# Performance work log

Hardware: AMD Instinct MI355X
Metric: run time of the kernel (lower is better)

## Reference

```python
import jax, jax.numpy as jnp
import numpy as np

B, T, C, H, W = 4, 5, 512, 32, 32   # bt = B*T = 20
G = 32                              # GroupNorm groups
EPS = 1e-6


def group_norm(x, gamma, beta):
    # x: [N, C, H, W]; normalize per (group-channels, H, W)
    n, c, h, w = x.shape
    xg = x.reshape(n, G, c // G, h * w)
    mu = jnp.mean(xg, axis=(2, 3), keepdims=True)
    var = jnp.mean((xg - mu) ** 2, axis=(2, 3), keepdims=True)
    xn = ((xg - mu) * jax.lax.rsqrt(var + EPS)).reshape(n, c, h, w)
    return xn * gamma[None, :, None, None] + beta[None, :, None, None]


def conv1x1(x, w, b):
    # 1x1 conv == channel matmul. x: [N,C,H,W], w: [O,C], b: [O]
    return jnp.einsum('nchw,oc->nohw', x, w) + b[None, :, None, None]


def setup_inputs() -> dict:
    key = jax.random.key(0)
    ks = jax.random.split(key, 9)
    inp = {'x': jax.random.normal(ks[0], (B * T, C, H, W), jnp.float32)}
    for i, nm in enumerate(['wq', 'wk', 'wv', 'wo', 'wqt', 'wkt', 'wvt', 'wot']):
        inp[nm] = jax.random.normal(ks[i + 1], (C, C), jnp.float32) * 0.02
        inp['b' + nm[1:]] = jnp.zeros((C,), jnp.float32)
    inp['gamma_s'] = jnp.ones((C,), jnp.float32)
    inp['beta_s'] = jnp.zeros((C,), jnp.float32)
    inp['gamma_t'] = jnp.ones((C,), jnp.float32)
    inp['beta_t'] = jnp.zeros((C,), jnp.float32)
    return inp


def reference(x, wq, bq, wk, bk, wv, bv, wo, bo,
              wqt, bqt, wkt, bkt, wvt, bvt, wot, bot,
              gamma_s, beta_s, gamma_t, beta_t):
    scale = float(C) ** -0.5

    # ---- spatial attention (AttnBlock.forward) ----
    hn = group_norm(x, gamma_s, beta_s)
    q = conv1x1(hn, wq, bq).reshape(B * T, C, H * W)
    k = conv1x1(hn, wk, bk).reshape(B * T, C, H * W)
    v = conv1x1(hn, wv, bv).reshape(B * T, C, H * W)
    # scores [bt, hw_q, hw_k], softmax over keys
    att = jax.nn.softmax(jnp.einsum('bcq,bck->bqk', q, k) * scale, axis=2)
    hsp = jnp.einsum('bck,bqk->bcq', v, att).reshape(B * T, C, H, W)
    spatio = x + conv1x1(hsp, wo, bo)

    # ---- temporal attention across t=5 frames per pixel ----
    hn = group_norm(spatio, gamma_t, beta_t)
    q5 = conv1x1(hn, wqt, bqt).reshape(B, T, C, H, W)
    k5 = conv1x1(hn, wkt, bkt).reshape(B, T, C, H, W)
    v5 = conv1x1(hn, wvt, bvt).reshape(B, T, C, H, W)
    # per-pixel [t, t] attention, softmax over key-frame axis s
    att_t = jax.nn.softmax(jnp.einsum('btchw,bschw->bhwts', q5, k5) * scale, axis=-1)
    htp = jnp.einsum('bhwts,bschw->btchw', att_t, v5).reshape(B * T, C, H, W)

    # NOTE: residual is the ORIGINAL x (faithful to the source), not spatio
    return x + conv1x1(htp, wot, bot)
```

## Files before the change

### kernel.cpp

```cpp
#include <hip/hip_runtime.h>
#include <hip/hip_bf16.h>
#include <stdint.h>

typedef unsigned short u16;
typedef __attribute__((ext_vector_type(8))) short bf16x8;
typedef __attribute__((ext_vector_type(4))) float f32x4;

#define DI __device__ __forceinline__

DI float b2f(u16 u) { return __uint_as_float(((uint32_t)u) << 16); }
DI u16 f2b(float f) {
  uint32_t u = __float_as_uint(f);
  u += 0x7fff + ((u >> 16) & 1);
  return (u16)(u >> 16);
}

DI void gld_lds16(const u16* g, u16* l) {
  __builtin_amdgcn_global_load_lds((const __attribute__((address_space(1))) void*)g,
                                   (__attribute__((address_space(3))) void*)l,
                                   16, 0, 0);
}

__global__ __launch_bounds__(256)
void setup_wb(const float* __restrict__ w0, const float* __restrict__ w1,
              const float* __restrict__ w2, const float* __restrict__ w3,
              const float* __restrict__ w4, const float* __restrict__ w5,
              const float* __restrict__ w6, const float* __restrict__ w7,
              const float* __restrict__ b0, const float* __restrict__ b1,
              const float* __restrict__ b2, const float* __restrict__ b3,
              const float* __restrict__ b4, const float* __restrict__ b5,
              const float* __restrict__ b6, const float* __restrict__ b7,
              u16* __restrict__ dst, float* __restrict__ bdst)
{
  if (blockIdx.x >= 1032) {
    const int a = (blockIdx.x - 1032) * 256 + threadIdx.x;
    float acc = 0.f;
    for (int c = 0; c < 512; ++c) acc += w3[a * 512 + c] * b2[c];
    bdst[4096 + a] = acc;
    return;
  }
  if (blockIdx.x >= 1024) {
    const float* bs[8] = {b0, b1, b2, b3, b4, b5, b6, b7};
    const int a = blockIdx.x - 1024;
    const int i = threadIdx.x;
    bdst[a * 512 + i] = bs[a][i];
    bdst[a * 512 + i + 256] = bs[a][i + 256];
    return;
  }
  const float* srcs[8] = {w0, w1, w2, w3, w4, w5, w6, w7};
  const int mat = blockIdx.x >> 7;
  const int i = (((blockIdx.x & 127) << 8) + threadIdx.x) * 8;
  const float* s = srcs[mat];
  float4 a = *(const float4*)(s + i);
  float4 b = *(const float4*)(s + i + 4);
  alignas(16) u16 v[8] = {f2b(a.x), f2b(a.y), f2b(a.z), f2b(a.w),
                          f2b(b.x), f2b(b.y), f2b(b.z), f2b(b.w)};
  *(uint4*)(dst + (long)mat * 262144 + i) = *(const uint4*)v;
  if (mat == 2) {
    const int row = i >> 9, col = i & 511;
#pragma unroll
    for (int j = 0; j < 8; ++j) dst[8 * 262144 + (col + j) * 512 + row] = v[j];
  }
}

template<int OUTF32, int BIASMODE, int RESID>
__global__ __launch_bounds__(256)
void gemm_bt(const u16* __restrict__ A, long sA, long lda,
             const u16* __restrict__ B, long sB, long ldb,
             void* __restrict__ C, long sC,
             const float* __restrict__ bias,
             const float* __restrict__ resid, long sR,
             int N, int K, float alpha)
{
  __shared__ u16 lA[2 * 128 * 32];
  __shared__ u16 lB[2 * 128 * 32];
  const int t = threadIdx.x;
  const int lane = t & 63;
  const int wid = t >> 6;

  const int nx = gridDim.x;
  const int bid = blockIdx.y * nx + blockIdx.x;
  const int nper = (nx * gridDim.y) >> 3;
  const int nid = (bid & 7) * nper + (bid >> 3);
  const int m0 = (nid / nx) * 128, n0 = (nid % nx) * 128;

  const long bz = blockIdx.z;
  const u16* Ab = A + bz * sA;
  const u16* Bb = B + bz * sB;

  const int row = t >> 2;
  const int kc  = (((t & 3) ^ ((t >> 3) & 3)) << 3);

  f32x4 acc[4][4];
#pragma unroll
  for (int i = 0; i < 4; ++i)
#pragma unroll
    for (int j = 0; j < 4; ++j) acc[i][j] = (f32x4){0.f, 0.f, 0.f, 0.f};

  const int ml = lane & 15, qd = lane >> 4;
  const int koff = ((qd ^ ((ml >> 1) & 3)) << 3);
  const int wm = (wid >> 1) * 64, wn = (wid & 1) * 64;

  auto stage = [&](int bsel, int k0) {
    const u16* Ap = Ab + (long)(m0 + row) * lda + (k0 + kc);
    const u16* Bp = Bb + (long)(n0 + row) * ldb + (k0 + kc);
    u16* la = lA + bsel * 4096 + wid * 512;
    u16* lb = lB + bsel * 4096 + wid * 512;
    gld_lds16(Ap, la);
    gld_lds16(Ap + 64 * lda, la + 2048);
    gld_lds16(Bp, lb);
    gld_lds16(Bp + 64 * ldb, lb + 2048);
  };

  const int niter = K >> 5;
  stage(0, 0);
  for (int i = 0; i < niter; ++i) {
    __syncthreads();
    if (i + 1 < niter) stage((i + 1) & 1, (i + 1) << 5);
    const u16* la = lA + (i & 1) * 4096;
    const u16* lb = lB + (i & 1) * 4096;
    bf16x8 af[4], bfr[4];
#pragma unroll
    for (int x = 0; x < 4; ++x)
      af[x] = *(const bf16x8*)&la[(wm + x * 16 + ml) * 32 + koff];
#pragma unroll
    for (int y = 0; y < 4; ++y)
      bfr[y] = *(const bf16x8*)&lb[(wn + y * 16 + ml) * 32 + koff];
#pragma unroll
    for (int x = 0; x < 4; ++x)
#pragma unroll
      for (int y = 0; y < 4; ++y)
        acc[x][y] = __builtin_amdgcn_mfma_f32_16x16x32_bf16(af[x], bfr[y], acc[x][y], 0, 0, 0);
  }

  const long cb = bz * sC;
#pragma unroll
  for (int i = 0; i < 4; ++i) {
#pragma unroll
    for (int j = 0; j < 4; ++j) {
#pragma unroll
      for (int r = 0; r < 4; ++r) {
        int rr = m0 + wm + i * 16 + qd * 4 + r;
        int cc = n0 + wn + j * 16 + ml;
        float v = acc[i][j][r] * alpha;
        if (BIASMODE == 1) v += bias[rr];
        if (BIASMODE == 2) v += bias[cc];
        long idx = (long)rr * N + cc;
        if (RESID) v += resid[bz * sR + idx];
        if (OUTF32) ((float*)C)[cb + idx] = v;
        else        ((u16*)C)[cb + idx] = f2b(v);
      }
    }
  }
}

template<int OUTF32, int BIASMODE, int RESID>
__global__ __launch_bounds__(512, 2)
void gemm256(const u16* __restrict__ A, long sA, long lda,
             const u16* __restrict__ B, long sB, long ldb,
             void* __restrict__ C, long sC,
             const float* __restrict__ bias,
             const float* __restrict__ resid, long sR,
             int N, int K, float alpha)
{
  __shared__ u16 lA[4 * 8192];
  __shared__ u16 lB[4 * 8192];
  const int t = threadIdx.x;
  const int lane = t & 63, wid = t >> 6;
  const int wr = wid >> 2, wc = wid & 3;
  const int ml = lane & 15, qd = lane >> 4;

  const int nx = gridDim.x;
  const int bid = blockIdx.y * nx + blockIdx.x;
  const int nper = (nx * gridDim.y) >> 3;
  const int nid = (bid & 7) * nper + (bid >> 3);
  const int m0 = (nid / nx) * 256, n0 = (nid % nx) * 256;

  const long bz = blockIdx.z;
  const u16* Ab = A + bz * sA;
  const u16* Bb = B + bz * sB;

  const int sw = ((lane & 3) ^ ((lane >> 3) & 3)) << 3;
  const int srow = wid * 32 + (lane >> 2);
  const u16* ApS = Ab + (long)(m0 + srow) * lda + sw;
  const u16* BpS = Bb + (long)(n0 + srow) * ldb + sw;
  u16* lwA = lA + wid * 1024;
  u16* lwB = lB + wid * 1024;

  f32x4 acc[8][4];
#pragma unroll
  for (int i = 0; i < 8; ++i)
#pragma unroll
    for (int j = 0; j < 4; ++j) acc[i][j] = (f32x4){0.f, 0.f, 0.f, 0.f};

  const int NT = K >> 5;

  auto stageA = [&](int tk) {
    const int bo = (tk & 3) << 13;
    const u16* p = ApS + ((long)tk << 5);
    gld_lds16(p,              lwA + bo);
    gld_lds16(p + (lda << 4), lwA + bo + 512);
  };
  auto stageB = [&](int tk) {
    const int bo = (tk & 3) << 13;
    const u16* p = BpS + ((long)tk << 5);
    gld_lds16(p,              lwB + bo);
    gld_lds16(p + (ldb << 4), lwB + bo + 512);
  };

  const int koff = (qd ^ ((ml >> 1) & 3)) << 3;
  const int rAo = (wr * 128 + ml) * 32 + koff;
  const int rBo = (wc * 64 + ml) * 32 + koff;

  stageA(0); stageB(0); stageA(1); stageB(1); stageA(2); stageB(2);
  asm volatile("s_waitcnt vmcnt(8)" ::: "memory");
  __builtin_amdgcn_s_barrier();
  __builtin_amdgcn_sched_barrier(0);

  for (int tk = 0; tk < NT; ++tk) {
    const int bo = (tk & 3) << 13;
    const u16* pa = lA + bo + rAo;
    const u16* pb = lB + bo + rBo;
    bf16x8 bfr[4], af[4];

#pragma unroll
    for (int n = 0; n < 4; ++n) bfr[n] = *(const bf16x8*)(pb + n * 512);
#pragma unroll
    for (int m = 0; m < 4; ++m) af[m] = *(const bf16x8*)(pa + m * 512);
    if (tk + 3 < NT) stageA(tk + 3);
    __builtin_amdgcn_sched_barrier(0);
    __builtin_amdgcn_s_barrier();
    asm volatile("s_waitcnt lgkmcnt(0)" ::: "memory");
    __builtin_amdgcn_sched_barrier(0);
    __builtin_amdgcn_s_setprio(1);
#pragma unroll
    for (int m = 0; m < 4; ++m)
#pragma unroll
      for (int n = 0; n < 4; ++n)
        acc[m][n] = __builtin_amdgcn_mfma_f32_16x16x32_bf16(af[m], bfr[n], acc[m][n], 0, 0, 0);
    __builtin_amdgcn_s_setprio(0);
    __builtin_amdgcn_sched_barrier(0);
    __builtin_amdgcn_s_barrier();
    __builtin_amdgcn_sched_barrier(0);

#pragma unroll
    for (int m = 0; m < 4; ++m) af[m] = *(const bf16x8*)(pa + (m + 4) * 512);
    if (tk + 3 < NT) stageB(tk + 3);
    __builtin_amdgcn_sched_barrier(0);
    __builtin_amdgcn_s_barrier();
    asm volatile("s_waitcnt lgkmcnt(0)" ::: "memory");
    __builtin_amdgcn_sched_barrier(0);
    __builtin_amdgcn_s_setprio(1);
#pragma unroll
    for (int m = 0; m < 4; ++m)
#pragma unroll
      for (int n = 0; n < 4; ++n)
        acc[m + 4][n] = __builtin_amdgcn_mfma_f32_16x16x32_bf16(af[m], bfr[n], acc[m + 4][n], 0, 0, 0);
    __builtin_amdgcn_s_setprio(0);
    __builtin_amdgcn_sched_barrier(0);

    if (tk < NT - 1) {
      const int rem = NT - 2 - tk;
      if (rem >= 2)      asm volatile("s_waitcnt vmcnt(8)" ::: "memory");
      else if (rem == 1) asm volatile("s_waitcnt vmcnt(4)" ::: "memory");
      else               asm volatile("s_waitcnt vmcnt(0)" ::: "memory");
      __builtin_amdgcn_s_barrier();
      __builtin_amdgcn_sched_barrier(0);
    }
  }

  const long cb = bz * sC;
#pragma unroll
  for (int mt = 0; mt < 8; ++mt) {
#pragma unroll
    for (int nt = 0; nt < 4; ++nt) {
#pragma unroll
      for (int r = 0; r < 4; ++r) {
        int rr = m0 + wr * 128 + mt * 16 + qd * 4 + r;
        int cc = n0 + wc * 64 + nt * 16 + ml;
        float v = acc[mt][nt][r] * alpha;
        if (BIASMODE == 1) v += bias[rr];
        if (BIASMODE == 2) v += bias[cc];
        long idx = (long)rr * N + cc;
        if (RESID) v += resid[bz * sR + idx];
        if (OUTF32) ((float*)C)[cb + idx] = v;
        else        ((u16*)C)[cb + idx] = f2b(v);
      }
    }
  }
}

__global__ __launch_bounds__(256)
void groupnorm_f32(const float* __restrict__ x, const float* __restrict__ gamma,
                   const float* __restrict__ beta, u16* __restrict__ out)
{
  const int C = 512, HW = 1024;
  const int n = blockIdx.x >> 5, g = blockIdx.x & 31;
  const float* xg = x + ((long)n * C + g * 16) * HW;
  const int t = threadIdx.x;
  float s = 0.f, ss = 0.f;
  for (int ch = t; ch < 4096; ch += 256) {
    float4 u = *(const float4*)(xg + ch * 4);
    s += u.x + u.y + u.z + u.w;
    ss += u.x * u.x + u.y * u.y + u.z * u.z + u.w * u.w;
  }
#pragma unroll
  for (int off = 32; off > 0; off >>= 1) { s += __shfl_xor(s, off); ss += __shfl_xor(ss, off); }
  __shared__ float rs[4], rss[4];
  if ((t & 63) == 0) { rs[t >> 6] = s; rss[t >> 6] = ss; }
  __syncthreads();
  s  = rs[0] + rs[1] + rs[2] + rs[3];
  ss = rss[0] + rss[1] + rss[2] + rss[3];
  const float mu = s * (1.f / 16384.f);
  const float var = ss * (1.f / 16384.f) - mu * mu;
  const float rstd = rsqrtf(var + 1e-6f);
  float gm[16], bt[16];
#pragma unroll
  for (int i = 0; i < 16; ++i) {
    float ga = gamma[g * 16 + i];
    gm[i] = ga * rstd;
    bt[i] = beta[g * 16 + i] - mu * ga * rstd;
  }
  for (int p = t; p < 1024; p += 256) {
    alignas(16) u16 vals[16];
#pragma unroll
    for (int i = 0; i < 16; ++i)
      vals[i] = f2b(xg[(long)i * HW + p] * gm[i] + bt[i]);
    u16* dst = out + ((long)n * HW + p) * C + g * 16;
    *(uint4*)dst       = *(const uint4*)&vals[0];
    *(uint4*)(dst + 8) = *(const uint4*)&vals[8];
  }
}

__global__ __launch_bounds__(256)
void groupnorm_bf16(const u16* __restrict__ x, const float* __restrict__ gamma,
                    const float* __restrict__ beta, u16* __restrict__ out)
{
  const int C = 512, HW = 1024;
  const int n = blockIdx.x >> 5, g = blockIdx.x & 31;
  const u16* xg = x + ((long)n * C + g * 16) * HW;
  const int t = threadIdx.x;
  float s = 0.f, ss = 0.f;
  for (int ch = t; ch < 2048; ch += 256) {
    uint4 u = *(const uint4*)(xg + ch * 8);
    uint32_t w[4] = {u.x, u.y, u.z, u.w};
#pragma unroll
    for (int k = 0; k < 4; ++k) {
      float f0 = __uint_as_float(w[k] << 16);
      float f1 = __uint_as_float(w[k] & 0xffff0000u);
      s += f0 + f1; ss += f0 * f0 + f1 * f1;
    }
  }
#pragma unroll
  for (int off = 32; off > 0; off >>= 1) { s += __shfl_xor(s, off); ss += __shfl_xor(ss, off); }
  __shared__ float rs[4], rss[4];
  if ((t & 63) == 0) { rs[t >> 6] = s; rss[t >> 6] = ss; }
  __syncthreads();
  s  = rs[0] + rs[1] + rs[2] + rs[3];
  ss = rss[0] + rss[1] + rss[2] + rss[3];
  const float mu = s * (1.f / 16384.f);
  const float var = ss * (1.f / 16384.f) - mu * mu;
  const float rstd = rsqrtf(var + 1e-6f);
  float gm[16], bt[16];
#pragma unroll
  for (int i = 0; i < 16; ++i) {
    float ga = gamma[g * 16 + i];
    gm[i] = ga * rstd;
    bt[i] = beta[g * 16 + i] - mu * ga * rstd;
  }
  for (int p = t; p < 1024; p += 256) {
    alignas(16) u16 vals[16];
#pragma unroll
    for (int i = 0; i < 16; ++i)
      vals[i] = f2b(b2f(xg[(long)i * HW + p]) * gm[i] + bt[i]);
    u16* dst = out + ((long)n * HW + p) * C + g * 16;
    *(uint4*)dst       = *(const uint4*)&vals[0];
    *(uint4*)(dst + 8) = *(const uint4*)&vals[8];
  }
}

__global__ __launch_bounds__(256)
void softmax1024(u16* __restrict__ data)
{
  u16* row = data + (long)blockIdx.x * 1024;
  const int t = threadIdx.x;
  uint2 u = *(const uint2*)(row + t * 4);
  float v[4];
  v[0] = __uint_as_float(u.x << 16); v[1] = __uint_as_float(u.x & 0xffff0000u);
  v[2] = __uint_as_float(u.y << 16); v[3] = __uint_as_float(u.y & 0xffff0000u);
  float mx = fmaxf(fmaxf(v[0], v[1]), fmaxf(v[2], v[3]));
#pragma unroll
  for (int off = 32; off > 0; off >>= 1) mx = fmaxf(mx, __shfl_xor(mx, off));
  __shared__ float red[8];
  if ((t & 63) == 0) red[t >> 6] = mx;
  __syncthreads();
  mx = fmaxf(fmaxf(red[0], red[1]), fmaxf(red[2], red[3]));
  float e[4]; float s = 0.f;
#pragma unroll
  for (int k = 0; k < 4; ++k) { e[k] = __expf(v[k] - mx); s += e[k]; }
#pragma unroll
  for (int off = 32; off > 0; off >>= 1) s += __shfl_xor(s, off);
  if ((t & 63) == 0) red[4 + (t >> 6)] = s;
  __syncthreads();
  s = red[4] + red[5] + red[6] + red[7];
  float inv = 1.f / s;
  uint2 o;
  o.x = (uint32_t)f2b(e[0] * inv) | ((uint32_t)f2b(e[1] * inv) << 16);
  o.y = (uint32_t)f2b(e[2] * inv) | ((uint32_t)f2b(e[3] * inv) << 16);
  *(uint2*)(row + t * 4) = o;
}

__global__ __launch_bounds__(256)
void temporal_attn(const u16* __restrict__ qkv, u16* __restrict__ htp)
{
  const int t = threadIdx.x;
  const int wv = t >> 6, lane = t & 63;
  const int pix = blockIdx.x * 4 + wv;
  const int b = pix >> 10, p = pix & 1023;
  const long fs = 1024l * 1536;
  const long rowbase = ((long)b * 5 * 1024 + p) * 1536 + lane * 8;

  float qf[5][8], kf[5][8];
#pragma unroll
  for (int f = 0; f < 5; ++f) {
    bf16x8 qv = *(const bf16x8*)(qkv + rowbase + f * fs);
    bf16x8 kv = *(const bf16x8*)(qkv + rowbase + f * fs + 512);
#pragma unroll
    for (int u = 0; u < 8; ++u) { qf[f][u] = b2f((u16)qv[u]); kf[f][u] = b2f((u16)kv[u]); }
  }
  float sc[25];
#pragma unroll
  for (int i = 0; i < 5; ++i)
#pragma unroll
    for (int j = 0; j < 5; ++j) {
      float a = 0.f;
#pragma unroll
      for (int u = 0; u < 8; ++u) a += qf[i][u] * kf[j][u];
      sc[i * 5 + j] = a;
    }
#pragma unroll
  for (int m = 1; m < 64; m <<= 1)
#pragma unroll
    for (int s = 0; s < 25; ++s) sc[s] += __shfl_xor(sc[s], m);

  const float scale = 0.04419417382415922f;
  float att[5][5];
#pragma unroll
  for (int i = 0; i < 5; ++i) {
    float m = sc[i * 5];
#pragma unroll
    for (int j = 1; j < 5; ++j) m = fmaxf(m, sc[i * 5 + j]);
    float ssum = 0.f;
#pragma unroll
    for (int j = 0; j < 5; ++j) { att[i][j] = __expf((sc[i * 5 + j] - m) * scale); ssum += att[i][j]; }
    float inv = 1.f / ssum;
#pragma unroll
    for (int j = 0; j < 5; ++j) att[i][j] *= inv;
  }

  float of[5][8];
#pragma unroll
  for (int i = 0; i < 5; ++i)
#pragma unroll
    for (int u = 0; u < 8; ++u) of[i][u] = 0.f;
#pragma unroll
  for (int s = 0; s < 5; ++s) {
    bf16x8 vvv = *(const bf16x8*)(qkv + rowbase + s * fs + 1024);
#pragma unroll
    for (int u = 0; u < 8; ++u) {
      float vf = b2f((u16)vvv[u]);
#pragma unroll
      for (int i = 0; i < 5; ++i) of[i][u] += att[i][s] * vf;
    }
  }
  const long obase = ((long)b * 5 * 1024 + p) * 512 + lane * 8;
#pragma unroll
  for (int i = 0; i < 5; ++i) {
    alignas(16) u16 ob[8];
#pragma unroll
    for (int u = 0; u < 8; ++u) ob[u] = f2b(of[i][u]);
    *(uint4*)(htp + obase + i * 1024 * 512) = *(const uint4*)ob;
  }
}

extern "C" void kernel_launch(void* const* d_in, const int* in_sizes, int n_in,
                              void* d_out, int out_size, void* d_ws, size_t ws_size,
                              hipStream_t stream)
{
  const float* x   = (const float*)d_in[0];
  const float* wq  = (const float*)d_in[1];
  const float* bq  = (const float*)d_in[2];
  const float* wk  = (const float*)d_in[3];
  const float* bk  = (const float*)d_in[4];
  const float* wv  = (const float*)d_in[5];
  const float* bv  = (const float*)d_in[6];
  const float* wo  = (const float*)d_in[7];
  const float* bo  = (const float*)d_in[8];
  const float* wqt = (const float*)d_in[9];
  const float* bqt = (const float*)d_in[10];
  const float* wkt = (const float*)d_in[11];
  const float* bkt = (const float*)d_in[12];
  const float* wvt = (const float*)d_in[13];
  const float* bvt = (const float*)d_in[14];
  const float* wot = (const float*)d_in[15];
  const float* bot = (const float*)d_in[16];
  const float* gs  = (const float*)d_in[17];
  const float* bs  = (const float*)d_in[18];
  const float* gt  = (const float*)d_in[19];
  const float* btt = (const float*)d_in[20];

  const long U = 20l * 1024 * 512;
  u16* W0 = (u16*)d_ws;
  u16* W1 = W0 + U;
  u16* W3 = W0 + 3 * U;
  u16* W4 = W0 + 4 * U;
  u16* W6 = W0 + 6 * U;
  u16* W7 = W0 + 7 * U;
  u16* Wt = W0 + 8 * U;
  u16* wvT_b = Wt + 8 * 262144;
  u16* Wovs  = Wt + 9 * 262144;
  float* Bf = (float*)(Wt + 10 * 262144);
  u16* wo_b  = Wt + 3 * 262144;
  u16* wqt_b = Wt + 4 * 262144;
  u16* wot_b = Wt + 7 * 262144;

  const long S  = 524288;
  const long S2 = 1048576;
  const float scale = 0.04419417382415922f;
  dim3 blk(256);
  dim3 blk5(512);

  setup_wb<<<1034, blk, 0, stream>>>(wq, wk, wv, wo, wqt, wkt, wvt, wot,
                                     bq, bk, bv, bo, bqt, bkt, bvt, bot, Wt, Bf);

  gemm_bt<0, 0, 0><<<dim3(4, 4, 1), blk, 0, stream>>>(
      wo_b, 0, 512, wvT_b, 0, 512, Wovs, 0, nullptr, nullptr, 0, 512, 512, 1.f);

  groupnorm_f32<<<640, blk, 0, stream>>>(x, gs, bs, W0);
  gemm_bt<0, 2, 0><<<dim3(8, 160, 1), blk, 0, stream>>>(
      W0, 0, 512, Wt, 0, 512, W1, 0, Bf, nullptr, 0, 1024, 512, 1.f);
  gemm_bt<0, 1, 0><<<dim3(8, 4, 20), blk, 0, stream>>>(
      Wovs, 0, 512, W0, S, 512, W3, S, Bf + 4096, nullptr, 0, 1024, 512, 1.f);
  gemm_bt<0, 0, 0><<<dim3(8, 8, 20), blk, 0, stream>>>(
      W1, S2, 1024, W1 + 512, S2, 1024, W4, S2, nullptr, nullptr, 0, 1024, 512, scale);
  softmax1024<<<20480, blk, 0, stream>>>(W4);
  gemm_bt<0, 1, 1><<<dim3(8, 4, 20), blk, 0, stream>>>(
      W3, S, 1024, W4, S2, 1024, W6, S, Bf + 1536, x, S, 1024, 1024, 1.f);
  groupnorm_bf16<<<640, blk, 0, stream>>>(W6, gt, btt, W7);
  gemm256<0, 2, 0><<<dim3(6, 80, 1), blk5, 0, stream>>>(
      W7, 0, 512, wqt_b, 0, 512, W1, 0, Bf + 2048, nullptr, 0, 1536, 512, 1.f);
  temporal_attn<<<1024, blk, 0, stream>>>(W1, W0);
  gemm_bt<1, 1, 1><<<dim3(8, 4, 20), blk, 0, stream>>>(
      wot_b, 0, 512, W0, S, 512, (float*)d_out, S, Bf + 3584, x, S, 1024, 512, 1.f);
}
```

Baseline: 458.2 us.

## Fuse spatial softmax into score GEMM epilogue and defer normalization to PV GEMM

Drops the standalone softmax kernel. The score GEMM epilogue now writes exp(scaled score) and adds per-row sums into a zeroed stats buffer with atomics. The PV GEMM then multiplies each column by the reciprocal of its row sum. This removes a full read and write pass over the 20x1024x1024 attention matrix. It also moves the spatial residual add out of that GEMM and into a new groupnorm kernel that reads the fp32 input directly. The cost is a memset launch and atomic traffic, and dropping the max subtraction risks exp overflow when scores are large.

```diff
diff --git a/kernel.cpp b/kernel.cpp
--- a/kernel.cpp
+++ b/kernel.cpp
@@ -63,14 +63,14 @@
   }
 }
 
-template<int OUTF32, int BIASMODE, int RESID>
+template<int OUTF32, int BIASMODE, int RESID, int SMEXP, int COLSCALE>
 __global__ __launch_bounds__(256)
 void gemm_bt(const u16* __restrict__ A, long sA, long lda,
              const u16* __restrict__ B, long sB, long ldb,
              void* __restrict__ C, long sC,
              const float* __restrict__ bias,
              const float* __restrict__ resid, long sR,
-             int N, int K, float alpha)
+             int N, int K, float alpha, float* __restrict__ stats)
 {
   __shared__ u16 lA[2 * 128 * 32];
   __shared__ u16 lB[2 * 128 * 32];
@@ -133,6 +133,39 @@
         acc[x][y] = __builtin_amdgcn_mfma_f32_16x16x32_bf16(af[x], bfr[y], acc[x][y], 0, 0, 0);
   }
 
+  float inv[4];
+  if (COLSCALE) {
+#pragma unroll
+    for (int j = 0; j < 4; ++j)
+      inv[j] = 1.f / stats[bz * 1024 + n0 + wn + j * 16 + ml];
+  }
+  if (SMEXP) {
+    float rs[16];
+#pragma unroll
+    for (int s = 0; s < 16; ++s) rs[s] = 0.f;
+#pragma unroll
+    for (int i = 0; i < 4; ++i)
+#pragma unroll
+      for (int j = 0; j < 4; ++j)
+#pragma unroll
+        for (int r = 0; r < 4; ++r) {
+          float e = __expf(acc[i][j][r] * alpha);
+          acc[i][j][r] = e;
+          rs[i * 4 + r] += e;
+        }
+#pragma unroll
+    for (int m = 1; m < 16; m <<= 1)
+#pragma unroll
+      for (int s = 0; s < 16; ++s) rs[s] += __shfl_xor(rs[s], m);
+    if (ml == 0) {
+#pragma unroll
+      for (int i = 0; i < 4; ++i)
+#pragma unroll
+        for (int r = 0; r < 4; ++r)
+          atomicAdd(&stats[bz * 1024 + m0 + wm + i * 16 + qd * 4 + r], rs[i * 4 + r]);
+    }
+  }
+
   const long cb = bz * sC;
 #pragma unroll
   for (int i = 0; i < 4; ++i) {
@@ -142,7 +175,9 @@
       for (int r = 0; r < 4; ++r) {
         int rr = m0 + wm + i * 16 + qd * 4 + r;
         int cc = n0 + wn + j * 16 + ml;
-        float v = acc[i][j][r] * alpha;
+        float v = acc[i][j][r];
+        if (!SMEXP) v *= alpha;
+        if (COLSCALE) v *= inv[j];
         if (BIASMODE == 1) v += bias[rr];
         if (BIASMODE == 2) v += bias[cc];
         long idx = (long)rr * N + cc;
@@ -333,23 +368,27 @@
 }
 
 __global__ __launch_bounds__(256)
-void groupnorm_bf16(const u16* __restrict__ x, const float* __restrict__ gamma,
-                    const float* __restrict__ beta, u16* __restrict__ out)
+void groupnorm_resid(const u16* __restrict__ h, const float* __restrict__ x,
+                     const float* __restrict__ gamma,
+                     const float* __restrict__ beta, u16* __restrict__ out)
 {
   const int C = 512, HW = 1024;
   const int n = blockIdx.x >> 5, g = blockIdx.x & 31;
-  const u16* xg = x + ((long)n * C + g * 16) * HW;
+  const long base = ((long)n * C + g * 16) * HW;
+  const float* xg = x + base;
+  const u16*  hg = h + base;
   const int t = threadIdx.x;
   float s = 0.f, ss = 0.f;
-  for (int ch = t; ch < 2048; ch += 256) {
-    uint4 u = *(const uint4*)(xg + ch * 8);
-    uint32_t w[4] = {u.x, u.y, u.z, u.w};
-#pragma unroll
-    for (int k = 0; k < 4; ++k) {
-      float f0 = __uint_as_float(w[k] << 16);
-      float f1 = __uint_as_float(w[k] & 0xffff0000u);
-      s += f0 + f1; ss += f0 * f0 + f1 * f1;
-    }
+  for (int ch = t; ch < 4096; ch += 256) {
+    float4 u = *(const float4*)(xg + ch * 4);
+    uint2 hv = *(const uint2*)(hg + ch * 4);
+    float h0 = __uint_as_float(hv.x << 16);
+    float h1 = __uint_as_float(hv.x & 0xffff0000u);
+    float h2 = __uint_as_float(hv.y << 16);
+    float h3 = __uint_as_float(hv.y & 0xffff0000u);
+    float v0 = u.x + h0, v1 = u.y + h1, v2 = u.z + h2, v3 = u.w + h3;
+    s += v0 + v1 + v2 + v3;
+    ss += v0 * v0 + v1 * v1 + v2 * v2 + v3 * v3;
   }
 #pragma unroll
   for (int off = 32; off > 0; off >>= 1) { s += __shfl_xor(s, off); ss += __shfl_xor(ss, off); }
@@ -372,42 +411,11 @@
     alignas(16) u16 vals[16];
 #pragma unroll
     for (int i = 0; i < 16; ++i)
-      vals[i] = f2b(b2f(xg[(long)i * HW + p]) * gm[i] + bt[i]);
+      vals[i] = f2b((xg[(long)i * HW + p] + b2f(hg[(long)i * HW + p])) * gm[i] + bt[i]);
     u16* dst = out + ((long)n * HW + p) * C + g * 16;
     *(uint4*)dst       = *(const uint4*)&vals[0];
     *(uint4*)(dst + 8) = *(const uint4*)&vals[8];
   }
-}
-
-__global__ __launch_bounds__(256)
-void softmax1024(u16* __restrict__ data)
-{
-  u16* row = data + (long)blockIdx.x * 1024;
-  const int t = threadIdx.x;
-  uint2 u = *(const uint2*)(row + t * 4);
-  float v[4];
-  v[0] = __uint_as_float(u.x << 16); v[1] = __uint_as_float(u.x & 0xffff0000u);
-  v[2] = __uint_as_float(u.y << 16); v[3] = __uint_as_float(u.y & 0xffff0000u);
-  float mx = fmaxf(fmaxf(v[0], v[1]), fmaxf(v[2], v[3]));
-#pragma unroll
-  for (int off = 32; off > 0; off >>= 1) mx = fmaxf(mx, __shfl_xor(mx, off));
-  __shared__ float red[8];
-  if ((t & 63) == 0) red[t >> 6] = mx;
-  __syncthreads();
-  mx = fmaxf(fmaxf(red[0], red[1]), fmaxf(red[2], red[3]));
-  float e[4]; float s = 0.f;
-#pragma unroll
-  for (int k = 0; k < 4; ++k) { e[k] = __expf(v[k] - mx); s += e[k]; }
-#pragma unroll
-  for (int off = 32; off > 0; off >>= 1) s += __shfl_xor(s, off);
-  if ((t & 63) == 0) red[4 + (t >> 6)] = s;
-  __syncthreads();
-  s = red[4] + red[5] + red[6] + red[7];
-  float inv = 1.f / s;
-  uint2 o;
-  o.x = (uint32_t)f2b(e[0] * inv) | ((uint32_t)f2b(e[1] * inv) << 16);
-  o.y = (uint32_t)f2b(e[2] * inv) | ((uint32_t)f2b(e[3] * inv) << 16);
-  *(uint2*)(row + t * 4) = o;
 }
 
 __global__ __launch_bounds__(256)
@@ -520,6 +528,7 @@
   u16* wvT_b = Wt + 8 * 262144;
   u16* Wovs  = Wt + 9 * 262144;
   float* Bf = (float*)(Wt + 10 * 262144);
+  float* Stats = Bf + 8192;
   u16* wo_b  = Wt + 3 * 262144;
   u16* wqt_b = Wt + 4 * 262144;
   u16* wot_b = Wt + 7 * 262144;
@@ -532,24 +541,24 @@
 
   setup_wb<<<1034, blk, 0, stream>>>(wq, wk, wv, wo, wqt, wkt, wvt, wot,
                                      bq, bk, bv, bo, bqt, bkt, bvt, bot, Wt, Bf);
-
-  gemm_bt<0, 0, 0><<<dim3(4, 4, 1), blk, 0, stream>>>(
-      wo_b, 0, 512, wvT_b, 0, 512, Wovs, 0, nullptr, nullptr, 0, 512, 512, 1.f);
+  hipMemsetAsync(Stats, 0, 20 * 1024 * sizeof(float), stream);
+
+  gemm_bt<0, 0, 0, 0, 0><<<dim3(4, 4, 1), blk, 0, stream>>>(
+      wo_b, 0, 512, wvT_b, 0, 512, Wovs, 0, nullptr, nullptr, 0, 512, 512, 1.f, nullptr);
 
   groupnorm_f32<<<640, blk, 0, stream>>>(x, gs, bs, W0);
-  gemm_bt<0, 2, 0><<<dim3(8, 160, 1), blk, 0, stream>>>(
-      W0, 0, 512, Wt, 0, 512, W1, 0, Bf, nullptr, 0, 1024, 512, 1.f);
-  gemm_bt<0, 1, 0><<<dim3(8, 4, 20), blk, 0, stream>>>(
-      Wovs, 0, 512, W0, S, 512, W3, S, Bf + 4096, nullptr, 0, 1024, 512, 1.f);
-  gemm_bt<0, 0, 0><<<dim3(8, 8, 20), blk, 0, stream>>>(
-      W1, S2, 1024, W1 + 512, S2, 1024, W4, S2, nullptr, nullptr, 0, 1024, 512, scale);
-  softmax1024<<<20480, blk, 0, stream>>>(W4);
-  gemm_bt<0, 1, 1><<<dim3(8, 4, 20), blk, 0, stream>>>(
-      W3, S, 1024, W4, S2, 1024, W6, S, Bf + 1536, x, S, 1024, 1024, 1.f);
-  groupnorm_bf16<<<640, blk, 0, stream>>>(W6, gt, btt, W7);
+  gemm_bt<0, 2, 0, 0, 0><<<dim3(8, 160, 1), blk, 0, stream>>>(
+      W0, 0, 512, Wt, 0, 512, W1, 0, Bf, nullptr, 0, 1024, 512, 1.f, nullptr);
+  gemm_bt<0, 1, 0, 0, 0><<<dim3(8, 4, 20), blk, 0, stream>>>(
+      Wovs, 0, 512, W0, S, 512, W3, S, Bf + 4096, nullptr, 0, 1024, 512, 1.f, nullptr);
+  gemm_bt<0, 0, 0, 1, 0><<<dim3(8, 8, 20), blk, 0, stream>>>(
+      W1, S2, 1024, W1 + 512, S2, 1024, W4, S2, nullptr, nullptr, 0, 1024, 512, scale, Stats);
+  gemm_bt<0, 1, 0, 0, 1><<<dim3(8, 4, 20), blk, 0, stream>>>(
+      W3, S, 1024, W4, S2, 1024, W6, S, Bf + 1536, nullptr, 0, 1024, 1024, 1.f, Stats);
+  groupnorm_resid<<<640, blk, 0, stream>>>(W6, x, gt, btt, W7);
   gemm256<0, 2, 0><<<dim3(6, 80, 1), blk5, 0, stream>>>(
       W7, 0, 512, wqt_b, 0, 512, W1, 0, Bf + 2048, nullptr, 0, 1536, 512, 1.f);
   temporal_attn<<<1024, blk, 0, stream>>>(W1, W0);
-  gemm_bt<1, 1, 1><<<dim3(8, 4, 20), blk, 0, stream>>>(
-      wot_b, 0, 512, W0, S, 512, (float*)d_out, S, Bf + 3584, x, S, 1024, 512, 1.f);
-}
+  gemm_bt<1, 1, 1, 0, 0><<<dim3(8, 4, 20), blk, 0, stream>>>(
+      wot_b, 0, 512, W0, S, 512, (float*)d_out, S, Bf + 3584, x, S, 1024, 512, 1.f, nullptr);
+}
```

New measurement: 442.6 us. -3.4%, faster.
